# Optimization experiments

Hardware: AMD Instinct MI355X
Metric: run time of the kernel (lower is better)

The kernel has to match this reference:

```python
import jax, jax.numpy as jnp
import numpy as np

S, B, I, H, E = 2048, 64, 256, 512, 256


def setup_inputs() -> dict:
    key = jax.random.key(0)
    ks = jax.random.split(key, 3)
    scale_e = 1.0 / np.sqrt(H)
    scale_x = 1.0 / np.sqrt(I + E)
    return {
        "input_seq": jax.random.normal(ks[0], (S, B, I), dtype=jnp.float32),
        "h_0": jnp.zeros((B, H), dtype=jnp.float32),
        "m_0": jnp.zeros((B, E), dtype=jnp.float32),
        "W_embed": jax.random.normal(ks[1], (E, H), dtype=jnp.float32) * scale_e,
        "b_embed": jnp.zeros((E,), dtype=jnp.float32),
        "W_ih": jax.random.normal(ks[2], (H, I + E), dtype=jnp.float32) * scale_x,
        "b_ih": jnp.zeros((H,), dtype=jnp.float32),
    }


def reference(input_seq, h_0, m_0, W_embed, b_embed, W_ih, b_ih):
    # Custom RNN cell per step t:
    #   m_t = h_prev @ W_embed.T + b_embed          (embedding of previous hidden)
    #   h_t = tanh([x_t, m_prev] @ W_ih.T + b_ih)   (uses the LAGGED m_prev)
    def step(carry, x_t):
        h_prev, m_prev = carry
        m_t = h_prev @ W_embed.T + b_embed                     # [B, E]
        combined = jnp.concatenate([x_t, m_prev], axis=1)      # [B, I+E]
        h_t = jnp.tanh(combined @ W_ih.T + b_ih)               # [B, H]
        return (h_t, m_t), h_t

    (h_T, m_T), outputs = jax.lax.scan(step, (h_0, m_0), input_seq)
    return outputs, h_T, m_T
```

## Files before the change

kernel.cpp:

```cpp
#include <hip/hip_runtime.h>


#define S2    1024
#define OUT_HT 67108864
#define OUT_MT 67141632

typedef _Float16 half8 __attribute__((ext_vector_type(8)));
typedef float f32x4 __attribute__((ext_vector_type(4)));

#define OFF_W2F   0u
#define OFF_WXF   524288u
#define OFF_C2    786432u
#define OFF_AVE   788480u
#define OFF_AVO   919552u
#define OFF_MEMB  1050624u
#define OFF_HX    1116160u
#define OFF_CNT   1378304u

__global__ __launch_bounds__(256) void k_memb(const float* __restrict__ h0,
                                              const float* __restrict__ We,
                                              const float* __restrict__ be,
                                              float* __restrict__ memb) {
  __shared__ float hs[512];
  int b = blockIdx.x, e = threadIdx.x;
  for (int i = threadIdx.x; i < 512; i += 256) hs[i] = h0[b * 512 + i];
  __syncthreads();
  float acc = be[e];
  const float* wr = We + (size_t)e * 512;
  for (int h = 0; h < 512; ++h) acc += hs[h] * wr[h];
  memb[b * 256 + e] = acc;
}

__global__ __launch_bounds__(256) void k_prep(
    const float* __restrict__ We, const float* __restrict__ be,
    const float* __restrict__ Wih, const float* __restrict__ bih,
    const float* __restrict__ m0, const float* __restrict__ memb,
    _Float16* __restrict__ w2f, _Float16* __restrict__ wxf,
    float* __restrict__ c2, float* __restrict__ ave, float* __restrict__ avo,
    unsigned int* __restrict__ cnt) {
  int blk = blockIdx.x, tid = threadIdx.x;
  if (blk < 1024) {
    int idx = blk * 256 + tid;
    int k = idx & 511, n = idx >> 9;
    float acc = 0.f;
    for (int e = 0; e < 256; ++e)
      acc += We[e * 512 + k] * Wih[n * 512 + 256 + e];
    int ntile = n >> 4, nl = n & 15;
    int kch = k >> 5, kq = (k >> 3) & 3, ke = k & 7;
    int lane = kq * 16 + nl;
    w2f[(size_t)((ntile * 16 + kch) * 64 + lane) * 8 + ke] = (_Float16)acc;
  } else if (blk < 1536) {
    int idx = (blk - 1024) * 256 + tid;
    int k = idx & 255, n = idx >> 8;
    float v = Wih[n * 512 + k];
    int ntile = n >> 4, nl = n & 15;
    int kch = k >> 5, kq = (k >> 3) & 3, ke = k & 7;
    int lane = kq * 16 + nl;
    wxf[(size_t)((ntile * 8 + kch) * 64 + lane) * 8 + ke] = (_Float16)v;
  } else if (blk < 1538) {
    int j = (blk - 1536) * 256 + tid;
    float acc = bih[j];
    for (int e = 0; e < 256; ++e) acc += be[e] * Wih[j * 512 + 256 + e];
    c2[j] = acc;
  } else if (blk < 1666) {
    int i = blk - 1538;
    int b = i >> 1, j = (i & 1) * 256 + tid;
    float acc = bih[j];
    for (int e = 0; e < 256; ++e) acc += m0[b * 256 + e] * Wih[j * 512 + 256 + e];
    ave[b * 512 + j] = acc;
  } else if (blk < 1794) {
    int i = blk - 1666;
    int b = i >> 1, j = (i & 1) * 256 + tid;
    float acc = bih[j];
    for (int e = 0; e < 256; ++e) acc += memb[b * 256 + e] * Wih[j * 512 + 256 + e];
    avo[b * 512 + j] = acc;
  } else {
    if (tid < 64) cnt[tid] = 0u;
  }
}

__device__ inline float fast_tanh(float x) {
  float z = __expf(2.f * x);
  return 1.f - 2.f / (z + 1.f);
}

__global__ __launch_bounds__(256, 1) void k_main(
    const float* __restrict__ x,
    const _Float16* __restrict__ w2f, const _Float16* __restrict__ wxf,
    const float* __restrict__ c2, const float* __restrict__ ave,
    const float* __restrict__ avo, _Float16* __restrict__ hx,
    unsigned int* __restrict__ cnt, float* __restrict__ out) {
  __shared__ __align__(16) _Float16 ha[16 * 520];
  __shared__ __align__(16) _Float16 xl[2][16 * 264];

  const int tid = threadIdx.x;
  const int g = blockIdx.x & 7;
  const int w = blockIdx.x >> 3;
  const int wave = tid >> 6, lane = tid & 63;
  const int q = lane >> 4, nl = lane & 15;
  const int ntile = w * 4 + wave;
  const int j = (ntile << 4) + nl;

  half8 w2r[16];
#pragma unroll
  for (int kc = 0; kc < 16; ++kc)
    w2r[kc] = *(const half8*)(w2f + (size_t)((ntile * 16 + kc) * 64 + lane) * 8);
  half8 wxr[8];
#pragma unroll
  for (int kc = 0; kc < 8; ++kc)
    wxr[kc] = *(const half8*)(wxf + (size_t)((ntile * 8 + kc) * 64 + lane) * 8);

  const float c2l = c2[j];
  float av0[4];
#pragma unroll
  for (int r = 0; r < 4; ++r) {
    int m = q * 4 + r;
    av0[r] = (m < 8) ? ave[(g * 8 + m) * 512 + j] : avo[(g * 8 + (m & 7)) * 512 + j];
  }

  const int row = tid >> 4, seg = tid & 15;
  const int bb = g * 8 + (row & 7);

  {
    int t = (row >> 3);
    const float* xp = x + (size_t)(t * 64 + bb) * 256 + seg * 16;
    _Float16* dst = &xl[0][row * 264 + seg * 16];
#pragma unroll
    for (int i = 0; i < 16; ++i) dst[i] = (_Float16)xp[i];
  }
  __syncthreads();

  for (int s = 0; s < S2; ++s) {
    float xpre[16];
    if (s + 1 < S2) {
      int t = 2 * (s + 1) + (row >> 3);
      const float* xp = x + (size_t)(t * 64 + bb) * 256 + seg * 16;
#pragma unroll
      for (int i = 0; i < 4; ++i) {
        float4 v = *(const float4*)(xp + i * 4);
        xpre[i * 4 + 0] = v.x; xpre[i * 4 + 1] = v.y;
        xpre[i * 4 + 2] = v.z; xpre[i * 4 + 3] = v.w;
      }
    }

    f32x4 acc = {0.f, 0.f, 0.f, 0.f};

    if (s > 0) {
      if (tid == 0) {
        unsigned target = 8u * (unsigned)s;
        while (__hip_atomic_load(&cnt[g], __ATOMIC_RELAXED, __HIP_MEMORY_SCOPE_AGENT) < target)
          __builtin_amdgcn_s_sleep(1);
        __builtin_amdgcn_fence(__ATOMIC_ACQUIRE, "agent");
      }
      __syncthreads();
      const _Float16* src = hx + (size_t)((((s - 1) & 1) * 8 + g) * 16 + row) * 512;
      {
        _Float16* drow = &ha[row * 520];
#pragma unroll
        for (int i = 0; i < 4; ++i) {
          int idx = seg + 16 * i;
          *(float4*)(drow + idx * 8) = *(const float4*)(src + idx * 8);
        }
      }
      __syncthreads();
#pragma unroll
      for (int kc = 0; kc < 16; ++kc) {
        half8 a = *(const half8*)(&ha[nl * 520 + kc * 32 + q * 8]);
        acc = __builtin_amdgcn_mfma_f32_16x16x32_f16(a, w2r[kc], acc, 0, 0, 0);
      }
    }

#pragma unroll
    for (int kc = 0; kc < 8; ++kc) {
      half8 a = *(const half8*)(&xl[s & 1][nl * 264 + kc * 32 + q * 8]);
      acc = __builtin_amdgcn_mfma_f32_16x16x32_f16(a, wxr[kc], acc, 0, 0, 0);
    }

#pragma unroll
    for (int r = 0; r < 4; ++r) {
      int m = q * 4 + r;
      float pre = acc[r] + (s == 0 ? av0[r] : c2l);
      float h = fast_tanh(pre);
      int t = 2 * s + (m >> 3);
      int b = g * 8 + (m & 7);
      out[(size_t)(t * 64 + b) * 512 + j] = h;
      if (s == S2 - 1 && m >= 8) out[(size_t)OUT_HT + b * 512 + j] = h;
      hx[(size_t)(((s & 1) * 8 + g) * 16 + m) * 512 + j] = (_Float16)h;
    }

    if (s + 1 < S2) {
      _Float16* dst = &xl[(s + 1) & 1][row * 264 + seg * 16];
#pragma unroll
      for (int i = 0; i < 16; ++i) dst[i] = (_Float16)xpre[i];
    }

    __syncthreads();
    if (tid == 0)
      __hip_atomic_fetch_add(&cnt[g], 1u, __ATOMIC_RELEASE, __HIP_MEMORY_SCOPE_AGENT);
  }
}

__global__ __launch_bounds__(256) void k_mt(float* __restrict__ out,
                                            const float* __restrict__ We,
                                            const float* __restrict__ be) {
  __shared__ float hs[512];
  int b = blockIdx.x, e = threadIdx.x;
  const float* hrow = out + (size_t)(2046 * 64 + b) * 512;
  for (int i = threadIdx.x; i < 512; i += 256) hs[i] = hrow[i];
  __syncthreads();
  float acc = be[e];
  const float* wr = We + (size_t)e * 512;
  for (int h = 0; h < 512; ++h) acc += hs[h] * wr[h];
  out[(size_t)OUT_MT + b * 256 + e] = acc;
}

extern "C" void kernel_launch(void* const* d_in, const int* in_sizes, int n_in,
                              void* d_out, int out_size, void* d_ws, size_t ws_size,
                              hipStream_t stream) {
  const float* x   = (const float*)d_in[0];
  const float* h0  = (const float*)d_in[1];
  const float* m0  = (const float*)d_in[2];
  const float* We  = (const float*)d_in[3];
  const float* be  = (const float*)d_in[4];
  const float* Wih = (const float*)d_in[5];
  const float* bih = (const float*)d_in[6];
  float* out = (float*)d_out;
  char* ws = (char*)d_ws;

  _Float16* w2f = (_Float16*)(ws + OFF_W2F);
  _Float16* wxf = (_Float16*)(ws + OFF_WXF);
  float* c2   = (float*)(ws + OFF_C2);
  float* ave  = (float*)(ws + OFF_AVE);
  float* avo  = (float*)(ws + OFF_AVO);
  float* memb = (float*)(ws + OFF_MEMB);
  _Float16* hx = (_Float16*)(ws + OFF_HX);
  unsigned int* cnt = (unsigned int*)(ws + OFF_CNT);

  k_memb<<<64, 256, 0, stream>>>(h0, We, be, memb);
  k_prep<<<1795, 256, 0, stream>>>(We, be, Wih, bih, m0, memb, w2f, wxf, c2, ave, avo, cnt);
  k_main<<<64, 256, 0, stream>>>(x, w2f, wxf, c2, ave, avo, hx, cnt, out);
  k_mt<<<64, 256, 0, stream>>>(out, We, be);
}
```

Measured before the change: 4.562 ms.

## Precompute input projection in parallel and replace block barriers with per-wave flags

Adds a separate parallel MFMA kernel that computes x@Wx for all timesteps into the output buffer, so the recurrent kernel only reads a precomputed term instead of converting and multiplying x every step. The recurrent kernel drops its shared-memory staging and __syncthreads. Each wave now publishes a per-wave step flag with system-coherent stores and spins on the 32 flags of its group, then loads h directly from global memory into registers. It also splits the MFMA chain into four independent accumulators to shorten the dependency chain. The cost is an extra pass writing and re-reading the projection buffer, plus busy-spinning without sleep and relying on cache-bypassing inline-asm stores for correct ordering.

```diff
diff --git a/kernel.cpp b/kernel.cpp
--- a/kernel.cpp
+++ b/kernel.cpp
@@ -7,6 +7,7 @@
 
 typedef _Float16 half8 __attribute__((ext_vector_type(8)));
 typedef float f32x4 __attribute__((ext_vector_type(4)));
+typedef unsigned long long u64x2 __attribute__((ext_vector_type(2)));
 
 #define OFF_W2F   0u
 #define OFF_WXF   524288u
@@ -15,7 +16,7 @@
 #define OFF_AVO   919552u
 #define OFF_MEMB  1050624u
 #define OFF_HX    1116160u
-#define OFF_CNT   1378304u
+#define OFF_FLG   1378304u
 
 __global__ __launch_bounds__(256) void k_memb(const float* __restrict__ h0,
                                               const float* __restrict__ We,
@@ -37,7 +38,7 @@
     const float* __restrict__ m0, const float* __restrict__ memb,
     _Float16* __restrict__ w2f, _Float16* __restrict__ wxf,
     float* __restrict__ c2, float* __restrict__ ave, float* __restrict__ avo,
-    unsigned int* __restrict__ cnt) {
+    unsigned int* __restrict__ flg) {
   int blk = blockIdx.x, tid = threadIdx.x;
   if (blk < 1024) {
     int idx = blk * 256 + tid;
@@ -75,7 +76,51 @@
     for (int e = 0; e < 256; ++e) acc += memb[b * 256 + e] * Wih[j * 512 + 256 + e];
     avo[b * 512 + j] = acc;
   } else {
-    if (tid < 64) cnt[tid] = 0u;
+    flg[tid] = 0u;
+  }
+}
+
+__global__ __launch_bounds__(512, 1) void k_xw(const float* __restrict__ x,
+                                               const _Float16* __restrict__ wxf,
+                                               float* __restrict__ out) {
+  __shared__ _Float16 ha[128 * 264];
+  const int tid = threadIdx.x;
+  const int rowbase = blockIdx.x * 128;
+  {
+    int r0 = tid >> 2, cs = (tid & 3) * 64;
+    const float* xp = x + (size_t)(rowbase + r0) * 256 + cs;
+    _Float16* dp = ha + r0 * 264 + cs;
+#pragma unroll
+    for (int i = 0; i < 16; ++i) {
+      float4 v = *(const float4*)(xp + i * 4);
+      dp[i * 4 + 0] = (_Float16)v.x; dp[i * 4 + 1] = (_Float16)v.y;
+      dp[i * 4 + 2] = (_Float16)v.z; dp[i * 4 + 3] = (_Float16)v.w;
+    }
+  }
+  __syncthreads();
+  const int wv = tid >> 6, lane = tid & 63;
+  const int q = lane >> 4, nl = lane & 15;
+  half8 bfr[4][8];
+#pragma unroll
+  for (int nt = 0; nt < 4; ++nt)
+#pragma unroll
+    for (int kc = 0; kc < 8; ++kc)
+      bfr[nt][kc] = *(const half8*)(wxf + (size_t)((((4 * wv + nt) * 8 + kc) * 64 + lane)) * 8);
+  for (int ch = 0; ch < 8; ++ch) {
+    f32x4 acc[4] = {{0.f,0.f,0.f,0.f},{0.f,0.f,0.f,0.f},{0.f,0.f,0.f,0.f},{0.f,0.f,0.f,0.f}};
+#pragma unroll
+    for (int kc = 0; kc < 8; ++kc) {
+      half8 a = *(const half8*)(ha + (ch * 16 + nl) * 264 + kc * 32 + q * 8);
+#pragma unroll
+      for (int nt = 0; nt < 4; ++nt)
+        acc[nt] = __builtin_amdgcn_mfma_f32_16x16x32_f16(a, bfr[nt][kc], acc[nt], 0, 0, 0);
+    }
+    int row = rowbase + ch * 16 + q * 4;
+#pragma unroll
+    for (int nt = 0; nt < 4; ++nt)
+#pragma unroll
+      for (int r = 0; r < 4; ++r)
+        out[(size_t)(row + r) * 512 + wv * 64 + nt * 16 + nl] = acc[nt][r];
   }
 }
 
@@ -85,14 +130,10 @@
 }
 
 __global__ __launch_bounds__(256, 1) void k_main(
-    const float* __restrict__ x,
-    const _Float16* __restrict__ w2f, const _Float16* __restrict__ wxf,
-    const float* __restrict__ c2, const float* __restrict__ ave,
-    const float* __restrict__ avo, _Float16* __restrict__ hx,
-    unsigned int* __restrict__ cnt, float* __restrict__ out) {
-  __shared__ __align__(16) _Float16 ha[16 * 520];
-  __shared__ __align__(16) _Float16 xl[2][16 * 264];
-
+    const _Float16* __restrict__ w2f, const float* __restrict__ c2,
+    const float* __restrict__ ave, const float* __restrict__ avo,
+    _Float16* __restrict__ hx, unsigned int* __restrict__ flags,
+    float* __restrict__ out) {
   const int tid = threadIdx.x;
   const int g = blockIdx.x & 7;
   const int w = blockIdx.x >> 3;
@@ -105,10 +146,6 @@
 #pragma unroll
   for (int kc = 0; kc < 16; ++kc)
     w2r[kc] = *(const half8*)(w2f + (size_t)((ntile * 16 + kc) * 64 + lane) * 8);
-  half8 wxr[8];
-#pragma unroll
-  for (int kc = 0; kc < 8; ++kc)
-    wxr[kc] = *(const half8*)(wxf + (size_t)((ntile * 8 + kc) * 64 + lane) * 8);
 
   const float c2l = c2[j];
   float av0[4];
@@ -118,85 +155,70 @@
     av0[r] = (m < 8) ? ave[(g * 8 + m) * 512 + j] : avo[(g * 8 + (m & 7)) * 512 + j];
   }
 
-  const int row = tid >> 4, seg = tid & 15;
-  const int bb = g * 8 + (row & 7);
-
-  {
-    int t = (row >> 3);
-    const float* xp = x + (size_t)(t * 64 + bb) * 256 + seg * 16;
-    _Float16* dst = &xl[0][row * 264 + seg * 16];
-#pragma unroll
-    for (int i = 0; i < 16; ++i) dst[i] = (_Float16)xp[i];
-  }
-  __syncthreads();
+  const unsigned int* fp = flags + g * 32;
+  unsigned int* myflag = flags + g * 32 + w * 4 + wave;
+
+  const _Float16* hxl = hx + (size_t)(g * 16 + nl) * 512 + q * 8;
+  _Float16* hxs = hx + (size_t)(g * 16 + q * 4) * 512 + j;
+
+  float* outp[4];
+#pragma unroll
+  for (int r = 0; r < 4; ++r) {
+    int m = q * 4 + r;
+    outp[r] = out + (size_t)((m >> 3) * 64 + g * 8 + (m & 7)) * 512 + j;
+  }
+  float xwc[4];
+#pragma unroll
+  for (int r = 0; r < 4; ++r) xwc[r] = *outp[r];
 
   for (int s = 0; s < S2; ++s) {
-    float xpre[16];
-    if (s + 1 < S2) {
-      int t = 2 * (s + 1) + (row >> 3);
-      const float* xp = x + (size_t)(t * 64 + bb) * 256 + seg * 16;
-#pragma unroll
-      for (int i = 0; i < 4; ++i) {
-        float4 v = *(const float4*)(xp + i * 4);
-        xpre[i * 4 + 0] = v.x; xpre[i * 4 + 1] = v.y;
-        xpre[i * 4 + 2] = v.z; xpre[i * 4 + 3] = v.w;
+    f32x4 acc[4] = {{0.f,0.f,0.f,0.f},{0.f,0.f,0.f,0.f},{0.f,0.f,0.f,0.f},{0.f,0.f,0.f,0.f}};
+    if (s > 0) {
+      if (lane < 32) {
+        const unsigned int* f1 = fp + lane;
+        const unsigned int tgt = (unsigned int)s;
+        while (__hip_atomic_load(f1, __ATOMIC_RELAXED, __HIP_MEMORY_SCOPE_SYSTEM) < tgt) {}
       }
-    }
-
-    f32x4 acc = {0.f, 0.f, 0.f, 0.f};
-
-    if (s > 0) {
-      if (tid == 0) {
-        unsigned target = 8u * (unsigned)s;
-        while (__hip_atomic_load(&cnt[g], __ATOMIC_RELAXED, __HIP_MEMORY_SCOPE_AGENT) < target)
-          __builtin_amdgcn_s_sleep(1);
-        __builtin_amdgcn_fence(__ATOMIC_ACQUIRE, "agent");
+      __builtin_amdgcn_sched_barrier(0);
+      const _Float16* hb = hxl + (((s - 1) & 1) ? 65536 : 0);
+      half8 hr[16];
+#pragma unroll
+      for (int kc = 0; kc < 16; ++kc) {
+        const unsigned long long* p = (const unsigned long long*)(hb + kc * 32);
+        u64x2 t;
+        t.x = __hip_atomic_load(p,     __ATOMIC_RELAXED, __HIP_MEMORY_SCOPE_SYSTEM);
+        t.y = __hip_atomic_load(p + 1, __ATOMIC_RELAXED, __HIP_MEMORY_SCOPE_SYSTEM);
+        hr[kc] = __builtin_bit_cast(half8, t);
       }
-      __syncthreads();
-      const _Float16* src = hx + (size_t)((((s - 1) & 1) * 8 + g) * 16 + row) * 512;
-      {
-        _Float16* drow = &ha[row * 520];
-#pragma unroll
-        for (int i = 0; i < 4; ++i) {
-          int idx = seg + 16 * i;
-          *(float4*)(drow + idx * 8) = *(const float4*)(src + idx * 8);
-        }
-      }
-      __syncthreads();
-#pragma unroll
-      for (int kc = 0; kc < 16; ++kc) {
-        half8 a = *(const half8*)(&ha[nl * 520 + kc * 32 + q * 8]);
-        acc = __builtin_amdgcn_mfma_f32_16x16x32_f16(a, w2r[kc], acc, 0, 0, 0);
-      }
-    }
-
-#pragma unroll
-    for (int kc = 0; kc < 8; ++kc) {
-      half8 a = *(const half8*)(&xl[s & 1][nl * 264 + kc * 32 + q * 8]);
-      acc = __builtin_amdgcn_mfma_f32_16x16x32_f16(a, wxr[kc], acc, 0, 0, 0);
-    }
-
+#pragma unroll
+      for (int kc = 0; kc < 16; ++kc)
+        acc[kc & 3] = __builtin_amdgcn_mfma_f32_16x16x32_f16(hr[kc], w2r[kc], acc[kc & 3], 0, 0, 0);
+    }
+
+    _Float16* hsp = hxs + ((s & 1) ? 65536 : 0);
 #pragma unroll
     for (int r = 0; r < 4; ++r) {
-      int m = q * 4 + r;
-      float pre = acc[r] + (s == 0 ? av0[r] : c2l);
+      float pre = acc[0][r] + acc[1][r] + acc[2][r] + acc[3][r] + xwc[r] +
+                  (s == 0 ? av0[r] : c2l);
       float h = fast_tanh(pre);
-      int t = 2 * s + (m >> 3);
-      int b = g * 8 + (m & 7);
-      out[(size_t)(t * 64 + b) * 512 + j] = h;
-      if (s == S2 - 1 && m >= 8) out[(size_t)OUT_HT + b * 512 + j] = h;
-      hx[(size_t)(((s & 1) * 8 + g) * 16 + m) * 512 + j] = (_Float16)h;
-    }
-
-    if (s + 1 < S2) {
-      _Float16* dst = &xl[(s + 1) & 1][row * 264 + seg * 16];
-#pragma unroll
-      for (int i = 0; i < 16; ++i) dst[i] = (_Float16)xpre[i];
-    }
-
-    __syncthreads();
-    if (tid == 0)
-      __hip_atomic_fetch_add(&cnt[g], 1u, __ATOMIC_RELEASE, __HIP_MEMORY_SCOPE_AGENT);
+      *outp[r] = h;
+      if (s == S2 - 1 && q >= 2)
+        out[(size_t)OUT_HT + (g * 8 + ((q - 2) * 4 + r)) * 512 + j] = h;
+      unsigned int hv = (unsigned int)__builtin_bit_cast(unsigned short, (_Float16)h);
+      asm volatile("global_store_short %0, %1, off sc0 sc1"
+                   :: "v"(hsp + r * 512), "v"(hv) : "memory");
+    }
+    asm volatile("s_waitcnt vmcnt(0)" ::: "memory");
+    if (lane == 0) {
+      unsigned int sv = (unsigned int)(s + 1);
+      asm volatile("global_store_dword %0, %1, off sc0 sc1"
+                   :: "v"(myflag), "v"(sv) : "memory");
+    }
+#pragma unroll
+    for (int r = 0; r < 4; ++r) {
+      outp[r] += 65536;
+      if (s + 1 < S2) xwc[r] = *outp[r];
+    }
   }
 }
 
@@ -234,10 +256,11 @@
   float* avo  = (float*)(ws + OFF_AVO);
   float* memb = (float*)(ws + OFF_MEMB);
   _Float16* hx = (_Float16*)(ws + OFF_HX);
-  unsigned int* cnt = (unsigned int*)(ws + OFF_CNT);
+  unsigned int* flg = (unsigned int*)(ws + OFF_FLG);
 
   k_memb<<<64, 256, 0, stream>>>(h0, We, be, memb);
-  k_prep<<<1795, 256, 0, stream>>>(We, be, Wih, bih, m0, memb, w2f, wxf, c2, ave, avo, cnt);
-  k_main<<<64, 256, 0, stream>>>(x, w2f, wxf, c2, ave, avo, hx, cnt, out);
+  k_prep<<<1795, 256, 0, stream>>>(We, be, Wih, bih, m0, memb, w2f, wxf, c2, ave, avo, flg);
+  k_xw<<<1024, 512, 0, stream>>>(x, wxf, out);
+  k_main<<<64, 256, 0, stream>>>(w2f, c2, ave, avo, hx, flg, out);
   k_mt<<<64, 256, 0, stream>>>(out, We, be);
 }
```

Result: slower. 6.241 ms (+36.8%).
